# Performance work log

Hardware: AMD Instinct MI355X
Metric: run time of the kernel (lower is better)

Reference implementation:

```python
import jax, jax.numpy as jnp
import numpy as np

DIM_CODES = 64
BOOK_SIZE = 1024
EMBED_DIM = 64
DECAY = 0.999
GAIN = 1.0 - DECAY
EPS = 1e-6


def setup_inputs() -> dict:
    key = jax.random.key(0)
    k1, k2 = jax.random.split(key)
    batch, cw_dim = 512, DIM_CODES * EMBED_DIM
    x = jax.random.normal(k1, (batch, cw_dim), dtype=jnp.float32)
    codebook = jax.random.normal(k2, (DIM_CODES, BOOK_SIZE, EMBED_DIM), dtype=jnp.float32)
    ema_counts = jnp.ones((DIM_CODES, BOOK_SIZE), dtype=jnp.float32)
    return {"x": x, "codebook": codebook, "ema_counts": ema_counts}


def reference(x, codebook, ema_counts):
    """VQVAE.quantise in training mode with EMA codebook update.

    x: [B, dim_codes*embed]; codebook: [D, K, E]; ema_counts: [D, K].
    Returns (cw, one_hot_idx, new_codebook, new_ema_counts).
    """
    B = x.shape[0]
    xr = x.reshape(B, DIM_CODES, EMBED_DIM)  # [B, D, E]

    x_sq = jnp.sum(xr * xr, axis=-1, keepdims=True)            # [B, D, 1]
    b_sq = jnp.sum(codebook * codebook, axis=-1)               # [D, K]
    xb = jnp.einsum('bde,dke->bdk', xr, codebook)              # [B, D, K]
    dist = x_sq - 2.0 * xb + b_sq[None, :, :]

    idx = jnp.argmin(dist, axis=-1)                            # [B, D] int

    # gather nearest code: cw_embed[b,d,:] = codebook[d, idx[b,d], :]
    cw_embed = jnp.take_along_axis(
        codebook[None], idx[:, :, None, None], axis=2
    )[:, :, 0, :]                                              # [B, D, E]

    one_hot_idx = jax.nn.one_hot(idx, BOOK_SIZE, dtype=x.dtype)  # [B, D, K]

    # EMA update (training): scatter-sum of x into assigned codes
    update_dict = jnp.einsum('bdk,bde->dke', one_hot_idx, xr)  # [D, K, E]
    normalize = ema_counts[:, :, None]                          # old counts
    new_codebook = codebook * DECAY + GAIN * update_dict / (normalize + EPS)
    new_ema_counts = DECAY * ema_counts + GAIN * jnp.sum(one_hot_idx, axis=0)

    # straight-through output (TransferGrad): forward value is cw_embed
    cw = x + jax.lax.stop_gradient(cw_embed.reshape(B, -1) - x)
    return cw, one_hot_idx, new_codebook, new_ema_counts
```

## Files before the change

### kernel.cpp

```cpp
#include <hip/hip_runtime.h>

#define DECAYF 0.999f
#define GAINF  0.001f
#define EPSF   1e-6f


#define NB 512
#define ND 64
#define NK 1024
#define NE 64

__global__ void k_pre(const float* __restrict__ cb, const float* __restrict__ ema,
                      float* __restrict__ ncb, float* __restrict__ nema) {
    int i = blockIdx.x * blockDim.x + threadIdx.x;
    if (i < 1048576) {
        float4 v = ((const float4*)cb)[i];
        v.x *= DECAYF; v.y *= DECAYF; v.z *= DECAYF; v.w *= DECAYF;
        ((float4*)ncb)[i] = v;
    } else {
        int j = i - 1048576;
        float4 v = ((const float4*)ema)[j];
        v.x *= DECAYF; v.y *= DECAYF; v.z *= DECAYF; v.w *= DECAYF;
        ((float4*)nema)[j] = v;
    }
}

__global__ __launch_bounds__(1024) void k_fused(
        const float* __restrict__ x, const float* __restrict__ cb,
        const float* __restrict__ ema,
        float* __restrict__ cw, float* __restrict__ oh,
        float* __restrict__ ncb, float* __restrict__ nema) {
    const int d    = blockIdx.x;
    const int bq   = blockIdx.y;
    const int t    = threadIdx.x;
    const int lane = t & 63;
    const int w    = __builtin_amdgcn_readfirstlane(t >> 6);

    __shared__ float s_hbsq[NK];
    __shared__ float s_best[16][64];
    __shared__ int   s_idx[16][64];
    __shared__ int   s_kf[64];
    __shared__ int   s_cnt[NK];

    s_cnt[t] = 0;

    const float* cbd = cb + (size_t)d * (NK * NE);
    {
        const float4* c4a = (const float4*)(cbd + (size_t)t * NE);
        float a0 = 0.f, a1 = 0.f, a2 = 0.f, a3 = 0.f;
#pragma unroll
        for (int e4 = 0; e4 < 16; ++e4) {
            float4 v = c4a[e4];
            a0 = fmaf(v.x, v.x, a0); a1 = fmaf(v.y, v.y, a1);
            a2 = fmaf(v.z, v.z, a2); a3 = fmaf(v.w, v.w, a3);
        }
        s_hbsq[t] = 0.5f * ((a0 + a1) + (a2 + a3));
    }
    __syncthreads();

    const int b = bq * 64 + lane;
    float4 xr[16];
    const float4* xp4 = (const float4*)(x + (size_t)b * (ND * NE) + d * NE);
#pragma unroll
    for (int e4 = 0; e4 < 16; ++e4) xr[e4] = xp4[e4];

    const float* crow = cbd + (size_t)(w * 64) * NE;
    const float* bsqw = s_hbsq + w * 64;
    float best  = 3.4e38f;
    int   bestk = w * 64;
    for (int k = 0; k < 64; ++k) {
        float a0 = 0.f, a1 = 0.f, a2 = 0.f, a3 = 0.f;
#pragma unroll
        for (int e = 0; e < 64; e += 4) {
            a0 = fmaf(crow[e],     xr[e >> 2].x, a0);
            a1 = fmaf(crow[e + 1], xr[e >> 2].y, a1);
            a2 = fmaf(crow[e + 2], xr[e >> 2].z, a2);
            a3 = fmaf(crow[e + 3], xr[e >> 2].w, a3);
        }
        crow += NE;
        float dist = bsqw[k] - ((a0 + a1) + (a2 + a3));
        if (dist < best) { best = dist; bestk = w * 64 + k; }
    }
    s_best[w][lane] = best;
    s_idx[w][lane]  = bestk;
    __syncthreads();

    if (t < 64) {
        float bv = s_best[0][t];
        int   bk = s_idx[0][t];
#pragma unroll
        for (int j = 1; j < 16; ++j) {
            float ob = s_best[j][t];
            if (ob < bv) { bv = ob; bk = s_idx[j][t]; }
        }
        s_kf[t] = bk;
        atomicAdd(&s_cnt[bk], 1);
    }
    __syncthreads();

    for (int rr = 0; rr < 4; ++rr) {
        int r  = w * 4 + rr;
        int kk = s_kf[r];
        float* orow = oh + (size_t)(bq * 64 + r) * (ND * NK) + d * NK;
#pragma unroll
        for (int j = 0; j < 4; ++j) {
            int k0 = j * 256 + lane * 4;
            float4 o;
            o.x = (k0     == kk) ? 1.f : 0.f;
            o.y = (k0 + 1 == kk) ? 1.f : 0.f;
            o.z = (k0 + 2 == kk) ? 1.f : 0.f;
            o.w = (k0 + 3 == kk) ? 1.f : 0.f;
            *(float4*)(orow + k0) = o;
        }
    }

    for (int rr = 0; rr < 4; ++rr) {
        int r  = w * 4 + rr;
        int kk = s_kf[r];
        int br = bq * 64 + r;
        float xv = x[(size_t)br * (ND * NE) + d * NE + lane];
        float cv = cbd[(size_t)kk * NE + lane];
        cw[(size_t)br * (ND * NE) + d * NE + lane] = xv + (cv - xv);
        float scale = GAINF / (ema[d * NK + kk] + EPSF);
        atomicAdd(&ncb[(size_t)d * (NK * NE) + (size_t)kk * NE + lane], scale * xv);
    }

    {
        int c = s_cnt[t];
        if (c) atomicAdd(&nema[d * NK + t], GAINF * (float)c);
    }
}

extern "C" void kernel_launch(void* const* d_in, const int* in_sizes, int n_in,
                              void* d_out, int out_size, void* d_ws, size_t ws_size,
                              hipStream_t stream) {
    const float* x   = (const float*)d_in[0];
    const float* cb  = (const float*)d_in[1];
    const float* ema = (const float*)d_in[2];
    (void)d_ws; (void)ws_size;

    float* out  = (float*)d_out;
    float* cw   = out;
    float* oh   = out + 2097152;
    float* ncb  = out + 2097152 + 33554432;
    float* nema = ncb + 4194304;

    k_pre<<<4160, 256, 0, stream>>>(cb, ema, ncb, nema);

    dim3 g_fused(64, 8);
    k_fused<<<g_fused, 1024, 0, stream>>>(x, cb, ema, cw, oh, ncb, nema);
}
```

Baseline: 271.0 us.

## Hold codebook rows in registers and reduce argmin across lanes with shuffles

The distance loop is remapped so each lane keeps one codebook row (64 floats) in registers, and the wave iterates over the 64 batch rows. The x values it reads are wave-uniform loads, and the per-row argmin is done with xor-shuffles on an order-preserving unsigned encoding of the distance, followed by a ballot to recover the index. This drops the shared b_sq table and the scattered per-lane codebook-row reads, in exchange for a 64-step shuffle reduction per batch row and higher register pressure. The launch bound now requests 4 blocks per multiprocessor.

```diff
diff --git a/kernel.cpp b/kernel.cpp
--- a/kernel.cpp
+++ b/kernel.cpp
@@ -25,7 +25,7 @@
     }
 }
 
-__global__ __launch_bounds__(1024) void k_fused(
+__global__ __launch_bounds__(1024, 4) void k_fused(
         const float* __restrict__ x, const float* __restrict__ cb,
         const float* __restrict__ ema,
         float* __restrict__ cw, float* __restrict__ oh,
@@ -36,62 +36,68 @@
     const int lane = t & 63;
     const int w    = __builtin_amdgcn_readfirstlane(t >> 6);
 
-    __shared__ float s_hbsq[NK];
-    __shared__ float s_best[16][64];
-    __shared__ int   s_idx[16][64];
-    __shared__ int   s_kf[64];
-    __shared__ int   s_cnt[NK];
+    __shared__ unsigned int s_ub[16][64];
+    __shared__ int          s_ix[16][64];
+    __shared__ int          s_kf[64];
+    __shared__ int          s_cnt[NK];
 
     s_cnt[t] = 0;
 
     const float* cbd = cb + (size_t)d * (NK * NE);
+    float c_reg[64];
     {
-        const float4* c4a = (const float4*)(cbd + (size_t)t * NE);
+        const float4* crow4 = (const float4*)(cbd + ((size_t)(w * 64) + lane) * NE);
+#pragma unroll
+        for (int e4 = 0; e4 < 16; ++e4) {
+            float4 v = crow4[e4];
+            c_reg[e4 * 4 + 0] = v.x; c_reg[e4 * 4 + 1] = v.y;
+            c_reg[e4 * 4 + 2] = v.z; c_reg[e4 * 4 + 3] = v.w;
+        }
+    }
+    float h0 = 0.f, h1 = 0.f, h2 = 0.f, h3 = 0.f;
+#pragma unroll
+    for (int e = 0; e < 64; e += 4) {
+        h0 = fmaf(c_reg[e],     c_reg[e],     h0);
+        h1 = fmaf(c_reg[e + 1], c_reg[e + 1], h1);
+        h2 = fmaf(c_reg[e + 2], c_reg[e + 2], h2);
+        h3 = fmaf(c_reg[e + 3], c_reg[e + 3], h3);
+    }
+    const float hb = 0.5f * ((h0 + h1) + (h2 + h3));
+
+    for (int b = 0; b < 64; ++b) {
+        const float* xrow = x + (size_t)(bq * 64 + b) * (ND * NE) + d * NE;
         float a0 = 0.f, a1 = 0.f, a2 = 0.f, a3 = 0.f;
 #pragma unroll
-        for (int e4 = 0; e4 < 16; ++e4) {
-            float4 v = c4a[e4];
-            a0 = fmaf(v.x, v.x, a0); a1 = fmaf(v.y, v.y, a1);
-            a2 = fmaf(v.z, v.z, a2); a3 = fmaf(v.w, v.w, a3);
+        for (int e = 0; e < 64; e += 4) {
+            a0 = fmaf(xrow[e],     c_reg[e],     a0);
+            a1 = fmaf(xrow[e + 1], c_reg[e + 1], a1);
+            a2 = fmaf(xrow[e + 2], c_reg[e + 2], a2);
+            a3 = fmaf(xrow[e + 3], c_reg[e + 3], a3);
         }
-        s_hbsq[t] = 0.5f * ((a0 + a1) + (a2 + a3));
+        float dist = hb - ((a0 + a1) + (a2 + a3));
+        unsigned int u = __float_as_uint(dist);
+        u = (u & 0x80000000u) ? ~u : (u | 0x80000000u);
+        const unsigned int u0 = u;
+#pragma unroll
+        for (int m = 1; m < 64; m <<= 1) {
+            unsigned int o = (unsigned int)__shfl_xor((int)u, m, 64);
+            u = (o < u) ? o : u;
+        }
+        unsigned long long eq = __ballot(u0 == u);
+        if (lane == 0) {
+            s_ub[w][b] = u;
+            s_ix[w][b] = w * 64 + (int)__builtin_ctzll(eq);
+        }
     }
     __syncthreads();
 
-    const int b = bq * 64 + lane;
-    float4 xr[16];
-    const float4* xp4 = (const float4*)(x + (size_t)b * (ND * NE) + d * NE);
-#pragma unroll
-    for (int e4 = 0; e4 < 16; ++e4) xr[e4] = xp4[e4];
-
-    const float* crow = cbd + (size_t)(w * 64) * NE;
-    const float* bsqw = s_hbsq + w * 64;
-    float best  = 3.4e38f;
-    int   bestk = w * 64;
-    for (int k = 0; k < 64; ++k) {
-        float a0 = 0.f, a1 = 0.f, a2 = 0.f, a3 = 0.f;
-#pragma unroll
-        for (int e = 0; e < 64; e += 4) {
-            a0 = fmaf(crow[e],     xr[e >> 2].x, a0);
-            a1 = fmaf(crow[e + 1], xr[e >> 2].y, a1);
-            a2 = fmaf(crow[e + 2], xr[e >> 2].z, a2);
-            a3 = fmaf(crow[e + 3], xr[e >> 2].w, a3);
-        }
-        crow += NE;
-        float dist = bsqw[k] - ((a0 + a1) + (a2 + a3));
-        if (dist < best) { best = dist; bestk = w * 64 + k; }
-    }
-    s_best[w][lane] = best;
-    s_idx[w][lane]  = bestk;
-    __syncthreads();
-
     if (t < 64) {
-        float bv = s_best[0][t];
-        int   bk = s_idx[0][t];
+        unsigned int bv = s_ub[0][t];
+        int bk = s_ix[0][t];
 #pragma unroll
         for (int j = 1; j < 16; ++j) {
-            float ob = s_best[j][t];
-            if (ob < bv) { bv = ob; bk = s_idx[j][t]; }
+            unsigned int ob = s_ub[j][t];
+            if (ob < bv) { bv = ob; bk = s_ix[j][t]; }
         }
         s_kf[t] = bk;
         atomicAdd(&s_cnt[bk], 1);
```

After: 383.2 us. +41.4%, slower.
